# Performance work log

Measured on AMD Instinct MI355X. Metric: run time of the kernel, lower is better.

The kernel has to match this reference:

```python
import jax, jax.numpy as jnp
import numpy as np

H, DH, DIM = 8, 64, 512
GAMMA, LAMBDA_REG = 0.01, 0.001


def setup_inputs() -> dict:
    key = jax.random.key(0)
    ks = jax.random.split(key, 12)
    Q, N = 4, 1024
    f = lambda k, shape, s=0.02: jax.random.normal(k, shape, dtype=jnp.float32) * s
    return {
        "q": jax.random.normal(ks[0], (Q, N, DIM), dtype=jnp.float32),
        "k": jax.random.normal(ks[1], (Q, N, DIM), dtype=jnp.float32),
        "v": jax.random.normal(ks[2], (Q, N, DIM), dtype=jnp.float32),
        "ln_w": jnp.ones((DIM,), jnp.float32),
        "ln_b": jnp.zeros((DIM,), jnp.float32),
        "W_in": f(ks[3], (DIM, H * DH)),
        "W_out": f(ks[4], (H * DH, DIM)),
        "b_out": jnp.zeros((DIM,), jnp.float32),
        "wp_W1": f(ks[5], (2 * DH, 4 * DH), 0.05),
        "wp_b1": jnp.zeros((4 * DH,), jnp.float32),
        "wp_ln_w": jnp.ones((4 * DH,), jnp.float32),
        "wp_ln_b": jnp.zeros((4 * DH,), jnp.float32),
        "wp_W2": f(ks[6], (4 * DH, 3 * DH), 0.05),
        "wp_b2": jnp.zeros((3 * DH,), jnp.float32),
        "wp_W3": f(ks[7], (3 * DH, DH), 0.05),
        "wp_b3": jnp.zeros((DH,), jnp.float32),
        "wp_W4": f(ks[8], (DH, 3), 0.05),
        "wp_b4": jnp.zeros((3,), jnp.float32),
        "weight_temp": jnp.ones((1,), jnp.float32) * 0.1,
    }


def _layernorm(x, w, b, eps=1e-5):
    mu = x.mean(-1, keepdims=True)
    var = x.var(-1, keepdims=True)  # biased, matches torch LayerNorm
    return (x - mu) / jnp.sqrt(var + eps) * w + b


def reference(q, k, v, ln_w, ln_b, W_in, W_out, b_out,
              wp_W1, wp_b1, wp_ln_w, wp_ln_b, wp_W2, wp_b2,
              wp_W3, wp_b3, wp_W4, wp_b4, weight_temp):
    # input_linear: LN -> Linear(no bias) -> (dropout=identity in eval)
    def proj(t):
        x = _layernorm(t, ln_w, ln_b) @ W_in  # [Q, N, H*DH]
        Qn, Nn = x.shape[0], x.shape[1]
        return x.reshape(Qn, Nn, H, DH).transpose(2, 0, 1, 3)  # h q n d

    fq, fk, fv = proj(q), proj(k), proj(v)
    m = fk.shape[2]

    # --- cosine component (cosine_distance + extra clamp) ---
    raw = jnp.einsum('hqnd,hqmd->hqnm', fq, fk)
    n1 = jnp.linalg.norm(fq, axis=-1)[..., :, None] + 1e-6
    n2 = jnp.linalg.norm(fk, axis=-1)[..., None, :] + 1e-6
    cosine_sim = jnp.clip(raw / (n1 * n2), -0.95, 0.95)

    # --- regularized covariance component ---
    fkc = fk - fk.mean(axis=2, keepdims=True)       # center keys over token dim
    fqc = fq - fq.mean(axis=-1, keepdims=True)      # center queries over feature dim
    cov = jnp.einsum('hqnd,hqmd->hqnm', fqc, fkc) / (DH ** 0.5 + 1e-4)
    cov = jnp.clip((LAMBDA_REG / max(m, 1)) * cov, -50.0, 50.0)

    # --- margin-based variance component (eval: adaptive_gamma = gamma) ---
    fqn = fq / jnp.maximum(jnp.linalg.norm(fq, axis=-1, keepdims=True), 1e-4)
    fkn = fk / jnp.maximum(jnp.linalg.norm(fk, axis=-1, keepdims=True), 1e-4)
    cs = jnp.clip(jnp.einsum('hqnd,hqmd->hqnm', fqn, fkn), -0.95, 0.95)
    margin = jnp.clip(GAMMA - cs, 0.0, 15.0)
    var_comp = jnp.broadcast_to(margin.mean(-1, keepdims=True), cs.shape)

    # --- dynamic per-head weights via MLP predictor ---
    feat = jnp.concatenate([fq.mean(axis=(1, 2)), fk.mean(axis=(1, 2))], axis=-1)  # (h, 2*DH)
    h1 = jax.nn.relu(_layernorm(feat @ wp_W1 + wp_b1, wp_ln_w, wp_ln_b))
    h2 = jax.nn.relu(h1 @ wp_W2 + wp_b2)
    h3 = jax.nn.relu(h2 @ wp_W3 + wp_b3)
    probs = jax.nn.softmax(h3 @ wp_W4 + wp_b4, axis=-1)  # predictor ends in Softmax
    wt = jnp.clip(weight_temp, 0.01, 1.0)
    w = jax.nn.softmax(probs / wt, axis=-1)
    w = jnp.clip(w, 0.01, 0.95)
    w = w / w.sum(-1, keepdims=True)
    cos_w = w[:, 0].reshape(H, 1, 1, 1)
    cov_w = w[:, 1].reshape(H, 1, 1, 1)
    var_w = w[:, 2].reshape(H, 1, 1, 1)

    # --- std-normalized weighted combination (torch.std is unbiased, detached) ---
    sg = jax.lax.stop_gradient
    ustd = lambda x: jnp.std(x, ddof=1)
    dots = (cos_w * (cosine_sim / (sg(ustd(cosine_sim)) + 1e-4))
            + cov_w * (cov / (sg(ustd(cov)) + 1e-4) * 0.3)
            + var_w * (var_comp / (sg(ustd(var_comp)) + 1e-4) * 0.3))

    ds = ustd(dots)  # NOT detached in original
    temp = jnp.where(ds < 1e-5, 0.01, jnp.where(ds < 1e-3, 0.05, 0.2 + ds * 2.0))
    temp = jnp.clip(temp, 0.01, 8.0)

    attn = jax.nn.softmax(dots / temp, axis=-1)
    out = jnp.einsum('hqnm,hqmd->hqnd', attn, fv)
    out = out.transpose(1, 2, 0, 3).reshape(out.shape[1], out.shape[2], H * DH)  # q n (h d)
    return out @ W_out + b_out
```

## Files before the change

kernel.cpp:

```cpp
#include <hip/hip_runtime.h>
#include <math.h>

typedef _Float16 f16;
typedef _Float16 v8h __attribute__((ext_vector_type(8)));
typedef _Float16 v4h __attribute__((ext_vector_type(4)));
typedef float    v4f __attribute__((ext_vector_type(4)));

#define MFMA(a, b, c) __builtin_amdgcn_mfma_f32_16x16x32_f16((a), (b), (c), 0, 0, 0)

#define OFF_LN16    0u
#define OFF_FQ16    4194304u
#define OFF_FK16    5242880u
#define OFF_FVHT    6291456u
#define OFF_WINTH   8388608u
#define OFF_WOUTTH  8650752u
#define OFF_AVH     8912896u
#define OFF_AVL     9961472u
#define OFF_RQ1     11010048u
#define OFF_RQ2     11042816u
#define OFF_MUQ     11075584u
#define OFF_RK1     11108352u
#define OFF_RK2     11141120u
#define OFF_SK      11173888u
#define OFF_VC      11206656u
#define OFF_ROWCOS  11272192u
#define OFF_ROWCOV  11337728u
#define OFF_NUACC   11403264u
#define OFF_PB      11405312u
#define OFF_HS      11411456u
#define OFF_RP      11411520u
#define OFF_FEAT    11411712u
#define OFF_WV      11412736u
#define OFF_SCAL    11412760u
#define OFF_MAXC    11412768u
#define OFF_MAXV    11478304u

__device__ __forceinline__ float clampf(float x, float lo, float hi) {
    return fminf(fmaxf(x, lo), hi);
}

__global__ void k_zero(float* feat, float* nuacck) {
    int i = blockIdx.x * 256 + threadIdx.x;
    if (i < 1024) feat[i] = 0.0f;
    if (i < 2048) nuacck[i] = 0.0f;
}

__global__ __launch_bounds__(256) void k_wprep(const float* __restrict__ Win,
        const float* __restrict__ Wout, f16* __restrict__ WinTh,
        f16* __restrict__ WoutTh) {
    __shared__ float lds[64][68];
    const float* W = blockIdx.z ? Wout : Win;
    f16* Th = blockIdx.z ? WoutTh : WinTh;
    int k0 = blockIdx.y * 64, c0 = blockIdx.x * 64;
    int t = threadIdx.x;
    #pragma unroll
    for (int p = 0; p < 4; ++p) {
        int flat = p * 1024 + t * 4;
        int r = flat >> 6, c = flat & 63;
        *(float4*)&lds[r][c] = *(const float4*)&W[(size_t)(k0 + r) * 512 + c0 + c];
    }
    __syncthreads();
    int c = t >> 2, kk = (t & 3) * 16;
    #pragma unroll
    for (int half = 0; half < 2; ++half) {
        v8h h8;
        #pragma unroll
        for (int ii = 0; ii < 8; ++ii)
            h8[ii] = (f16)lds[kk + half * 8 + ii][c];
        *(v8h*)&Th[(size_t)(c0 + c) * 512 + k0 + kk + half * 8] = h8;
    }
}

__global__ __launch_bounds__(256) void k_ln16(const float* __restrict__ q,
        const float* __restrict__ kk, const float* __restrict__ v,
        const float* __restrict__ lnw, const float* __restrict__ lnb,
        f16* __restrict__ ln16) {
    int t = threadIdx.x, wid = t >> 6, lane = t & 63;
    int token = blockIdx.x * 4 + wid;
    int inp = token >> 12, lt = token & 4095;
    const float* xp = (inp == 0) ? q : ((inp == 1) ? kk : v);
    const float4* xr = (const float4*)(xp + (size_t)lt * 512);
    float4 a = xr[lane], b = xr[lane + 64];
    float s = a.x + a.y + a.z + a.w + b.x + b.y + b.z + b.w;
    float s2 = a.x*a.x + a.y*a.y + a.z*a.z + a.w*a.w
             + b.x*b.x + b.y*b.y + b.z*b.z + b.w*b.w;
    for (int o = 32; o > 0; o >>= 1) { s += __shfl_down(s, o); s2 += __shfl_down(s2, o); }
    float m_ = __shfl(s, 0) * (1.0f / 512.0f);
    float var = __shfl(s2, 0) * (1.0f / 512.0f) - m_ * m_;
    var = fmaxf(var, 0.0f);
    float rs = rsqrtf(var + 1e-5f);
    const float4* w4 = (const float4*)lnw;
    const float4* b4 = (const float4*)lnb;
    float4 wa = w4[lane], wb = w4[lane + 64], ba = b4[lane], bb = b4[lane + 64];
    f16* orow = ln16 + (size_t)token * 512;
    v4h ha, hb;
    ha[0] = (f16)((a.x - m_) * rs * wa.x + ba.x);
    ha[1] = (f16)((a.y - m_) * rs * wa.y + ba.y);
    ha[2] = (f16)((a.z - m_) * rs * wa.z + ba.z);
    ha[3] = (f16)((a.w - m_) * rs * wa.w + ba.w);
    hb[0] = (f16)((b.x - m_) * rs * wb.x + bb.x);
    hb[1] = (f16)((b.y - m_) * rs * wb.y + bb.y);
    hb[2] = (f16)((b.z - m_) * rs * wb.z + bb.z);
    hb[3] = (f16)((b.w - m_) * rs * wb.w + bb.w);
    *(v4h*)&orow[lane * 4] = ha;
    *(v4h*)&orow[lane * 4 + 256] = hb;
}

template<int MODE>
__device__ __forceinline__ void proj_body(const f16* __restrict__ A16,
        const f16* __restrict__ BTh,
        f16* __restrict__ fout16, f16* __restrict__ fhT,
        float* __restrict__ oA, float* __restrict__ oB, float* __restrict__ oC,
        float* __restrict__ feat, float* __restrict__ nuacck) {
    int t = threadIdx.x, l = t & 63, w = t >> 6;
    int wr = w >> 1, wc = w & 1;
    int col0 = blockIdx.x * 128 + wc * 64;
    int tok0 = blockIdx.y * 128 + wr * 64;
    int lr = l & 15, kg = (l >> 4) * 8;
    int rg4 = (l >> 4) * 4;
    v4f acc[4][4] = {};
    for (int ks = 0; ks < 512; ks += 32) {
        v8h a[4], b[4];
        #pragma unroll
        for (int i = 0; i < 4; ++i)
            a[i] = *(const v8h*)&A16[(size_t)(tok0 + i * 16 + lr) * 512 + ks + kg];
        #pragma unroll
        for (int j = 0; j < 4; ++j)
            b[j] = *(const v8h*)&BTh[(size_t)(col0 + j * 16 + lr) * 512 + ks + kg];
        #pragma unroll
        for (int i = 0; i < 4; ++i)
            #pragma unroll
            for (int j = 0; j < 4; ++j)
                acc[i][j] = MFMA(a[i], b[j], acc[i][j]);
    }
    int h = col0 >> 6;
    #pragma unroll
    for (int i = 0; i < 4; ++i)
        #pragma unroll
        for (int j = 0; j < 4; ++j)
            #pragma unroll
            for (int r = 0; r < 4; ++r) {
                int token = tok0 + i * 16 + rg4 + r;
                int d = j * 16 + lr;
                int qi = token >> 10, n = token & 1023;
                float val = acc[i][j][r];
                if constexpr (MODE != 2) {
                    fout16[((size_t)((h << 2) + qi) * 1024 + n) * 64 + d] = (f16)val;
                } else {
                    fhT[((size_t)((h << 2) + qi) * 64 + d) * 1024 + n] = (f16)val;
                }
            }
    if constexpr (MODE != 2) {
        #pragma unroll
        for (int i = 0; i < 4; ++i)
            #pragma unroll
            for (int r = 0; r < 4; ++r) {
                float s = 0.f, s2 = 0.f;
                #pragma unroll
                for (int j = 0; j < 4; ++j) { float v = acc[i][j][r]; s += v; s2 += v * v; }
                #pragma unroll
                for (int mk = 1; mk <= 8; mk <<= 1) {
                    s += __shfl_xor(s, mk); s2 += __shfl_xor(s2, mk);
                }
                if (lr == 0) {
                    int token = tok0 + i * 16 + rg4 + r;
                    int qi = token >> 10, n = token & 1023;
                    int row = ((h << 2) + qi) * 1024 + n;
                    float nv = sqrtf(s2);
                    oA[row] = 1.0f / (nv + 1e-6f);
                    oB[row] = 1.0f / fmaxf(nv, 1e-4f);
                    oC[row] = (MODE == 0) ? s * (1.0f / 64.0f) : s;
                }
            }
        float cs[4];
        #pragma unroll
        for (int j = 0; j < 4; ++j) {
            float c = 0.f;
            #pragma unroll
            for (int i = 0; i < 4; ++i)
                #pragma unroll
                for (int r = 0; r < 4; ++r) c += acc[i][j][r];
            c += __shfl_xor(c, 16); c += __shfl_xor(c, 32);
            cs[j] = c;
        }
        if (l < 16) {
            #pragma unroll
            for (int j = 0; j < 4; ++j)
                atomicAdd(&feat[h * 128 + (MODE == 1 ? 64 : 0) + j * 16 + l],
                          cs[j] * (1.0f / 4096.0f));
            if constexpr (MODE == 1) {
                int qi = tok0 >> 10;
                #pragma unroll
                for (int j = 0; j < 4; ++j)
                    atomicAdd(&nuacck[((h << 2) + qi) * 64 + j * 16 + l], cs[j]);
            }
        }
    }
}

__global__ __launch_bounds__(256) void k_proj_all(const f16* __restrict__ ln16,
        const f16* __restrict__ BTh,
        f16* __restrict__ fq16, f16* __restrict__ fk16,
        f16* __restrict__ fvhT,
        float* __restrict__ rq1, float* __restrict__ rq2, float* __restrict__ muq,
        float* __restrict__ rk1, float* __restrict__ rk2, float* __restrict__ sk,
        float* __restrict__ feat, float* __restrict__ nuacck) {
    int mode = blockIdx.z;
    if (mode == 0)
        proj_body<0>(ln16, BTh, fq16, nullptr, rq1, rq2, muq, feat, nullptr);
    else if (mode == 1)
        proj_body<1>(ln16 + 2097152u, BTh, fk16, nullptr, rk1, rk2, sk, feat, nuacck);
    else
        proj_body<2>(ln16 + 4194304u, BTh, nullptr, fvhT,
                     nullptr, nullptr, nullptr, nullptr, nullptr);
}

__global__ __launch_bounds__(256) void k_mlp(const float* __restrict__ feat,
        const float* __restrict__ W1, const float* __restrict__ b1,
        const float* __restrict__ lw, const float* __restrict__ lb,
        const float* __restrict__ W2, const float* __restrict__ b2,
        const float* __restrict__ W3, const float* __restrict__ b3,
        const float* __restrict__ W4, const float* __restrict__ b4,
        const float* __restrict__ wtemp, float* wv) {
    __shared__ float h1[256], h2[192], h3[64], red[8];
    int t = threadIdx.x;
    int h = blockIdx.x;
    float p = 0.0f;
    for (int i = 0; i < 128; ++i) p += feat[h * 128 + i] * W1[i * 256 + t];
    p += b1[t];
    float s = p, s2 = p * p;
    for (int o = 32; o > 0; o >>= 1) { s += __shfl_down(s, o); s2 += __shfl_down(s2, o); }
    if ((t & 63) == 0) { red[t >> 6] = s; red[4 + (t >> 6)] = s2; }
    __syncthreads();
    float S = red[0] + red[1] + red[2] + red[3];
    float S2 = red[4] + red[5] + red[6] + red[7];
    float mu = S / 256.0f;
    float var = S2 / 256.0f - mu * mu; if (var < 0.0f) var = 0.0f;
    float xh = (p - mu) * rsqrtf(var + 1e-5f) * lw[t] + lb[t];
    h1[t] = fmaxf(xh, 0.0f);
    __syncthreads();
    if (t < 192) {
        float a = 0.0f;
        for (int i = 0; i < 256; ++i) a += h1[i] * W2[i * 192 + t];
        h2[t] = fmaxf(a + b2[t], 0.0f);
    }
    __syncthreads();
    if (t < 64) {
        float a = 0.0f;
        for (int i = 0; i < 192; ++i) a += h2[i] * W3[i * 64 + t];
        h3[t] = fmaxf(a + b3[t], 0.0f);
    }
    __syncthreads();
    if (t == 0) {
        float lg[3];
        for (int j = 0; j < 3; ++j) {
            float a = 0.0f;
            for (int i = 0; i < 64; ++i) a += h3[i] * W4[i * 3 + j];
            lg[j] = a + b4[j];
        }
        float mx = fmaxf(lg[0], fmaxf(lg[1], lg[2]));
        float e0 = expf(lg[0] - mx), e1 = expf(lg[1] - mx), e2 = expf(lg[2] - mx);
        float se = e0 + e1 + e2;
        float pr0 = e0 / se, pr1 = e1 / se, pr2 = e2 / se;
        float wt = wtemp[0]; wt = fminf(fmaxf(wt, 0.01f), 1.0f);
        float q0 = pr0 / wt, q1 = pr1 / wt, q2 = pr2 / wt;
        float m2 = fmaxf(q0, fmaxf(q1, q2));
        float f0 = expf(q0 - m2), f1 = expf(q1 - m2), f2 = expf(q2 - m2);
        float sf = f0 + f1 + f2; f0 /= sf; f1 /= sf; f2 /= sf;
        f0 = fminf(fmaxf(f0, 0.01f), 0.95f);
        f1 = fminf(fmaxf(f1, 0.01f), 0.95f);
        f2 = fminf(fmaxf(f2, 0.01f), 0.95f);
        float sw = f0 + f1 + f2;
        wv[h * 3 + 0] = f0 / sw; wv[h * 3 + 1] = f1 / sw; wv[h * 3 + 2] = f2 / sw;
    }
}

#define PASS_PREAMBLE_AB                                                       \
    int hq = blockIdx.z;                                                       \
    int half = blockIdx.y;                                                     \
    int m0base = half * 512;                                                   \
    int t = threadIdx.x, l = t & 63, w = t >> 6;                               \
    int lr = l & 15, kg = (l >> 4) * 8, rg4 = (l >> 4) * 4;                    \
    int nb = blockIdx.x * 64 + w * 16;                                         \
    const f16* Q = fq16 + (size_t)hq * 65536;                                  \
    const f16* K = fk16 + (size_t)hq * 65536;                                  \
    v8h aq0 = *(const v8h*)&Q[(size_t)(nb + lr) * 64 + kg];                    \
    v8h aq1 = *(const v8h*)&Q[(size_t)(nb + lr) * 64 + 32 + kg];               \
    const float inv1024 = 1.0f / 1024.0f;                                      \
    float uvp = nuacck[hq * 64 + l] * inv1024;                                 \
    _Pragma("unroll")                                                          \
    for (int o = 32; o > 0; o >>= 1) uvp += __shfl_xor(uvp, o);                \
    float uv = uvp;                                                            \
    float tp = 0.f;                                                            \
    _Pragma("unroll")                                                          \
    for (int e = 0; e < 8; ++e)                                                \
        tp += (float)aq0[e] * nuacck[hq * 64 + kg + e]                         \
            + (float)aq1[e] * nuacck[hq * 64 + 32 + kg + e];                   \
    tp *= inv1024;                                                             \
    tp += __shfl_xor(tp, 16);                                                  \
    tp += __shfl_xor(tp, 32);                                                  \
    float muv[4], tv[4];                                                       \
    _Pragma("unroll")                                                          \
    for (int r = 0; r < 4; ++r) {                                              \
        muv[r] = muq[hq * 1024 + nb + rg4 + r];                                \
        tv[r] = __shfl(tp, rg4 + r);                                           \
    }                                                                          \
    const float Acs = (0.001f / 1024.0f) / 8.0001f;                            \
    float Pr[4], Gr[4];                                                        \
    _Pragma("unroll")                                                          \
    for (int r = 0; r < 4; ++r) {                                              \
        Gr[r] = Acs * muv[r];                                                  \
        Pr[r] = Acs * fmaf(muv[r], uv, -tv[r]);                                \
    }

#define LOAD_KTILE(m0a)                                                        \
    v8h b0[4], b1[4];                                                          \
    _Pragma("unroll")                                                          \
    for (int j = 0; j < 4; ++j) {                                              \
        b0[j] = *(const v8h*)&K[(size_t)((m0a) + j * 16 + lr) * 64 + kg];      \
        b1[j] = *(const v8h*)&K[(size_t)((m0a) + j * 16 + lr) * 64 + 32 + kg]; \
    }

__global__ __launch_bounds__(256) void k_passA(const f16* __restrict__ fq16,
        const f16* __restrict__ fk16, const float* __restrict__ rq1,
        const float* __restrict__ rq2, const float* __restrict__ muq,
        const float* __restrict__ rk1, const float* __restrict__ rk2,
        const float* __restrict__ sk, const float* __restrict__ nuacck,
        float* __restrict__ vcrow, float* __restrict__ rowcos,
        float* __restrict__ rowcov, float* __restrict__ maxc,
        float* __restrict__ maxv, float* __restrict__ pb) {
    __shared__ float rk1s[512], rk2s[512], sks[512];
    PASS_PREAMBLE_AB
    {
        int i2 = t * 2;
        *(float2*)&rk1s[i2] = *(const float2*)&rk1[hq * 1024 + m0base + i2];
        *(float2*)&rk2s[i2] = *(const float2*)&rk2[hq * 1024 + m0base + i2];
        *(float2*)&sks[i2]  = *(const float2*)&sk[hq * 1024 + m0base + i2];
    }
    __syncthreads();
    float rq1v[4], rq2v[4];
    #pragma unroll
    for (int r = 0; r < 4; ++r) {
        rq1v[r] = rq1[hq * 1024 + nb + rg4 + r];
        rq2v[r] = rq2[hq * 1024 + nb + rg4 + r];
    }
    float scos = 0, s2cos = 0, scov = 0, s2cov = 0, sccov = 0;
    float mp[4] = {}, rcs[4] = {}, rcv[4] = {};
    float mcs[4] = { -1e30f, -1e30f, -1e30f, -1e30f };
    float mcv[4] = { -1e30f, -1e30f, -1e30f, -1e30f };
    #pragma unroll 2
    for (int m0 = 0; m0 < 512; m0 += 64) {
        LOAD_KTILE(m0base + m0)
        float rk1v[4], rk2v[4], skv[4];
        #pragma unroll
        for (int j = 0; j < 4; ++j) {
            int cg = m0 + j * 16 + lr;
            rk1v[j] = rk1s[cg]; rk2v[j] = rk2s[cg]; skv[j] = sks[cg];
        }
        v4f acc[4] = {};
        #pragma unroll
        for (int j = 0; j < 4; ++j) {
            acc[j] = MFMA(aq0, b0[j], acc[j]);
            acc[j] = MFMA(aq1, b1[j], acc[j]);
        }
        #pragma unroll
        for (int j = 0; j < 4; ++j)
            #pragma unroll
            for (int r = 0; r < 4; ++r) {
                float rv = acc[j][r];
                float cosv = clampf(rv * rq1v[r] * rk1v[j], -0.95f, 0.95f);
                float x2 = rv * rq2v[r] * rk2v[j];
                float marg = fmaxf(0.01f - fmaxf(x2, -0.95f), 0.0f);
                float cov = fmaf(-Gr[r], skv[j], fmaf(Acs, rv, Pr[r]));
                scos += cosv; s2cos = fmaf(cosv, cosv, s2cos);
                scov += cov;  s2cov = fmaf(cov, cov, s2cov);
                sccov = fmaf(cosv, cov, sccov);
                mp[r] += marg; rcs[r] += cosv; rcv[r] += cov;
                mcs[r] = fmaxf(mcs[r], cosv);
                mcv[r] = fmaxf(mcv[r], cov);
            }
    }
    #pragma unroll
    for (int r = 0; r < 4; ++r) {
        float m_ = mp[r], c_ = rcs[r], v_ = rcv[r];
        float xc = mcs[r], xv = mcv[r];
        #pragma unroll
        for (int mk = 1; mk <= 8; mk <<= 1) {
            m_ += __shfl_xor(m_, mk);
            c_ += __shfl_xor(c_, mk);
            v_ += __shfl_xor(v_, mk);
            xc = fmaxf(xc, __shfl_xor(xc, mk));
            xv = fmaxf(xv, __shfl_xor(xv, mk));
        }
        if (lr == 0) {
            int row = hq * 1024 + nb + rg4 + r;
            vcrow[half * 32768 + row] = m_ * inv1024;
            rowcos[half * 32768 + row] = c_;
            rowcov[half * 32768 + row] = v_;
            maxc[half * 32768 + row] = xc;
            maxv[half * 32768 + row] = xv;
        }
    }
    for (int o = 32; o > 0; o >>= 1) {
        scos += __shfl_down(scos, o); s2cos += __shfl_down(s2cos, o);
        scov += __shfl_down(scov, o); s2cov += __shfl_down(s2cov, o);
        sccov += __shfl_down(sccov, o);
    }
    __shared__ float bs[4][5];
    if (l == 0) { bs[w][0] = scos; bs[w][1] = s2cos; bs[w][2] = scov;
                  bs[w][3] = s2cov; bs[w][4] = sccov; }
    __syncthreads();
    if (t == 0) {
        int bid = (hq * 2 + half) * 16 + blockIdx.x;
        #pragma unroll
        for (int s = 0; s < 5; ++s)
            pb[bid * 6 + s] = bs[0][s] + bs[1][s] + bs[2][s] + bs[3][s];
    }
}

__global__ __launch_bounds__(256) void k_fin1(const float* __restrict__ pb,
        const float* __restrict__ vcrow, float* __restrict__ hs,
        float* __restrict__ scal) {
    __shared__ float hsl[40];
    int t = threadIdx.x;
    int hd = t >> 5, idx = t & 31;
    double a0 = 0, a1 = 0, a2 = 0, a3 = 0, a4 = 0;
    for (int i = idx; i < 128; i += 32) {
        const float* p = &pb[(hd * 128 + i) * 6];
        a0 += p[0]; a1 += p[1]; a2 += p[2]; a3 += p[3]; a4 += p[4];
    }
    for (int m = 1; m <= 16; m <<= 1) {
        a0 += __shfl_xor(a0, m); a1 += __shfl_xor(a1, m); a2 += __shfl_xor(a2, m);
        a3 += __shfl_xor(a3, m); a4 += __shfl_xor(a4, m);
    }
    if (idx == 0) {
        hsl[hd * 5 + 0] = (float)a0; hsl[hd * 5 + 1] = (float)a1;
        hsl[hd * 5 + 2] = (float)a2; hsl[hd * 5 + 3] = (float)a3;
        hsl[hd * 5 + 4] = (float)a4;
        hs[hd * 5 + 0] = (float)a0; hs[hd * 5 + 1] = (float)a1;
        hs[hd * 5 + 2] = (float)a2; hs[hd * 5 + 3] = (float)a3;
        hs[hd * 5 + 4] = (float)a4;
    }
    double s4 = 0, s5 = 0;
    for (int i = t; i < 32768; i += 256) {
        double rm = (double)(vcrow[i] + vcrow[32768 + i]);
        s4 += rm; s5 += rm * rm;
    }
    for (int o = 32; o > 0; o >>= 1) { s4 += __shfl_down(s4, o); s5 += __shfl_down(s5, o); }
    __shared__ double red[2][4];
    int wid = t >> 6, lane = t & 63;
    if (lane == 0) { red[0][wid] = s4; red[1][wid] = s5; }
    __syncthreads();
    if (t == 0) {
        double S4 = red[0][0] + red[0][1] + red[0][2] + red[0][3];
        double S5 = red[1][0] + red[1][1] + red[1][2] + red[1][3];
        double S0 = 0, S1 = 0, S2 = 0, S3 = 0;
        for (int h2 = 0; h2 < 8; ++h2) {
            S0 += hsl[h2 * 5 + 0]; S1 += hsl[h2 * 5 + 1];
            S2 += hsl[h2 * 5 + 2]; S3 += hsl[h2 * 5 + 3];
        }
        const double cnt = 33554432.0;
        scal[0] = (float)sqrt(fmax(0.0, (S1 - S0 * S0 / cnt) / (cnt - 1.0)));
        scal[1] = (float)sqrt(fmax(0.0, (S3 - S2 * S2 / cnt) / (cnt - 1.0)));
        double V4 = S4 * 1024.0, V5 = S5 * 1024.0;
        scal[2] = (float)sqrt(fmax(0.0, (V5 - V4 * V4 / cnt) / (cnt - 1.0)));
    }
}

__global__ __launch_bounds__(256) void k_finrow(const float* __restrict__ vcrow,
        const float* __restrict__ rowcos, const float* __restrict__ rowcov,
        const float* __restrict__ wv, const float* __restrict__ scal,
        float* __restrict__ rp) {
    int t = threadIdx.x;
    float s1 = scal[0] + 1e-4f, s2v = scal[1] + 1e-4f, s3 = scal[2] + 1e-4f;
    float p1 = 0, p2 = 0, p3 = 0;
    #pragma unroll
    for (int i = 0; i < 2; ++i) {
        int row = blockIdx.x * 512 + i * 256 + t;
        int h = row >> 12;
        float fc1 = wv[h * 3] / s1;
        float fc2 = wv[h * 3 + 1] * 0.3f / s2v;
        float c3 = wv[h * 3 + 2] * 0.3f / s3;
        float a = (vcrow[row] + vcrow[32768 + row]) * c3;
        float b = fc1 * (rowcos[row] + rowcos[32768 + row])
                + fc2 * (rowcov[row] + rowcov[32768 + row]);
        p1 += a; p2 = fmaf(a, a, p2); p3 = fmaf(a, b, p3);
    }
    for (int o = 32; o > 0; o >>= 1) {
        p1 += __shfl_down(p1, o); p2 += __shfl_down(p2, o); p3 += __shfl_down(p3, o);
    }
    __shared__ float red[3][4];
    int wid = t >> 6, lane = t & 63;
    if (lane == 0) { red[0][wid] = p1; red[1][wid] = p2; red[2][wid] = p3; }
    __syncthreads();
    if (t == 0) {
        rp[blockIdx.x * 3 + 0] = red[0][0] + red[0][1] + red[0][2] + red[0][3];
        rp[blockIdx.x * 3 + 1] = red[1][0] + red[1][1] + red[1][2] + red[1][3];
        rp[blockIdx.x * 3 + 2] = red[2][0] + red[2][1] + red[2][2] + red[2][3];
    }
}

__global__ __launch_bounds__(64) void k_fin2(const float* __restrict__ rp,
        const float* __restrict__ hs, const float* __restrict__ wv,
        float* __restrict__ scal) {
    int t = threadIdx.x;
    double p1 = rp[t * 3 + 0], p2 = rp[t * 3 + 1], p3 = rp[t * 3 + 2];
    for (int o = 32; o > 0; o >>= 1) {
        p1 += __shfl_down(p1, o); p2 += __shfl_down(p2, o); p3 += __shfl_down(p3, o);
    }
    if (t == 0) {
        double s1 = (double)scal[0] + 1e-4, s2v = (double)scal[1] + 1e-4;
        double sdd = 1024.0 * p1;
        double sdd2 = 2.0 * p3 + 1024.0 * p2;
        for (int h = 0; h < 8; ++h) {
            double fc1 = (double)wv[h * 3] / s1;
            double fc2 = (double)wv[h * 3 + 1] * 0.3 / s2v;
            sdd += fc1 * hs[h * 5 + 0] + fc2 * hs[h * 5 + 2];
            sdd2 += fc1 * fc1 * hs[h * 5 + 1] + fc2 * fc2 * hs[h * 5 + 3]
                  + 2.0 * fc1 * fc2 * hs[h * 5 + 4];
        }
        const double cnt = 33554432.0;
        double ds = sqrt(fmax(0.0, (sdd2 - sdd * sdd / cnt) / (cnt - 1.0)));
        float temp = (ds < 1e-5) ? 0.01f : ((ds < 1e-3) ? 0.05f : (0.2f + (float)ds * 2.0f));
        temp = fminf(fmaxf(temp, 0.01f), 8.0f);
        scal[3] = temp;
    }
}

#define TILE_STEP(PBASE, MK)                                                   \
    {                                                                          \
        int mk = (MK);                                                         \
        v8h b0[4], b1[4];                                                      \
        _Pragma("unroll")                                                      \
        for (int j = 0; j < 4; ++j) {                                          \
            b0[j] = *(const v8h*)&K[(size_t)(mk + j * 16 + lr) * 64 + kg];     \
            b1[j] = *(const v8h*)&K[(size_t)(mk + j * 16 + lr) * 64 + 32 + kg];\
        }                                                                      \
        float rk1v[4], skv[4];                                                 \
        _Pragma("unroll")                                                      \
        for (int j = 0; j < 4; ++j) {                                          \
            int cg = mk + j * 16 + lr;                                         \
            rk1v[j] = rk1s[cg]; skv[j] = sks[cg];                              \
        }                                                                      \
        v4f acc[4] = {};                                                       \
        _Pragma("unroll")                                                      \
        for (int j = 0; j < 4; ++j) {                                          \
            acc[j] = MFMA(aq0, b0[j], acc[j]);                                 \
            acc[j] = MFMA(aq1, b1[j], acc[j]);                                 \
        }                                                                      \
        _Pragma("unroll")                                                      \
        for (int j = 0; j < 4; ++j)                                            \
            _Pragma("unroll")                                                  \
            for (int r = 0; r < 4; ++r) {                                      \
                float rv = acc[j][r];                                          \
                float cosv = clampf(rv * rq1v[r] * rk1v[j], -0.95f, 0.95f);    \
                float cov = fmaf(-Gcr[r], skv[j], fmaf(Acs, rv, Pcr[r]));      \
                float d2 = fmaf(fc2, cov, fmaf(fc1, cosv, addc[r]));           \
                float pe = __expf(fmaf(d2, invt, -mxr[r]));                    \
                f16 p16 = (f16)pe;                                             \
                rsacc[r] += (float)p16;                                        \
                (PBASE)[(w * 16 + rg4 + r) * 72 + j * 16 + lr] = p16;          \
            }                                                                  \
        v8h pa0 = *(const v8h*)&(PBASE)[(w * 16 + lr) * 72 + kg];              \
        v8h pa1 = *(const v8h*)&(PBASE)[(w * 16 + lr) * 72 + 32 + kg];         \
        _Pragma("unroll")                                                      \
        for (int j = 0; j < 4; ++j) {                                          \
            size_t vb = ((size_t)hq * 64 + j * 16 + lr) * 1024 + mk;           \
            v8h vh0 = *(const v8h*)&fvhT[vb + kg];                             \
            v8h vh1 = *(const v8h*)&fvhT[vb + 32 + kg];                        \
            accpv[j] = MFMA(pa0, vh0, accpv[j]);                               \
            accpv[j] = MFMA(pa1, vh1, accpv[j]);                               \
        }                                                                      \
    }

__global__ __launch_bounds__(512) void k_passC(const f16* __restrict__ fq16,
        const f16* __restrict__ fk16, const float* __restrict__ rq1,
        const float* __restrict__ muq, const float* __restrict__ rk1,
        const float* __restrict__ sk, const float* __restrict__ nuacck,
        const float* __restrict__ vcrow, const float* __restrict__ maxca,
        const float* __restrict__ maxva, const float* __restrict__ wv,
        const float* __restrict__ scal,
        const f16* __restrict__ fvhT,
        f16* __restrict__ avh, f16* __restrict__ avl) {
    __shared__ __align__(16) char arena[36864];
    __shared__ float rk1s[1024], sks[1024];
    f16* Pa = (f16*)arena;
    f16* Pb = (f16*)(arena + 18432);
    int hq = blockIdx.y;
    int t = threadIdx.x, l = t & 63, w = t >> 6;
    int rg = w & 3, kh = w >> 2;
    int lr = l & 15, kg = (l >> 4) * 8, rg4 = (l >> 4) * 4;
    int nb = blockIdx.x * 64 + rg * 16;
    int m0base = kh * 512;
    const f16* Q = fq16 + (size_t)hq * 65536;
    const f16* K = fk16 + (size_t)hq * 65536;
    {
        int i2 = t * 2;
        *(float2*)&rk1s[i2] = *(const float2*)&rk1[hq * 1024 + i2];
        *(float2*)&sks[i2]  = *(const float2*)&sk[hq * 1024 + i2];
    }
    __syncthreads();
    v8h aq0 = *(const v8h*)&Q[(size_t)(nb + lr) * 64 + kg];
    v8h aq1 = *(const v8h*)&Q[(size_t)(nb + lr) * 64 + 32 + kg];
    const float inv1024 = 1.0f / 1024.0f;
    float uvp = nuacck[hq * 64 + l] * inv1024;
    #pragma unroll
    for (int o = 32; o > 0; o >>= 1) uvp += __shfl_xor(uvp, o);
    float uv = uvp;
    float tpv = 0.f;
    #pragma unroll
    for (int e = 0; e < 8; ++e)
        tpv += (float)aq0[e] * nuacck[hq * 64 + kg + e]
             + (float)aq1[e] * nuacck[hq * 64 + 32 + kg + e];
    tpv *= inv1024;
    tpv += __shfl_xor(tpv, 16);
    tpv += __shfl_xor(tpv, 32);
    float muv[4], tv[4];
    #pragma unroll
    for (int r = 0; r < 4; ++r) {
        muv[r] = muq[hq * 1024 + nb + rg4 + r];
        tv[r] = __shfl(tpv, rg4 + r);
    }
    const float Acs = (0.001f / 1024.0f) / 8.0001f;
    float Pcr[4], Gcr[4];
    #pragma unroll
    for (int r = 0; r < 4; ++r) {
        Gcr[r] = Acs * muv[r];
        Pcr[r] = Acs * fmaf(muv[r], uv, -tv[r]);
    }
    int h = hq >> 2;
    float s1 = scal[0] + 1e-4f, s2v = scal[1] + 1e-4f, s3 = scal[2] + 1e-4f;
    float fc1 = wv[h * 3] / s1;
    float fc2 = wv[h * 3 + 1] * 0.3f / s2v;
    float c3 = wv[h * 3 + 2] * 0.3f / s3;
    float invt = 1.0f / scal[3];
    float rq1v[4], addc[4], mxr[4];
    #pragma unroll
    for (int r = 0; r < 4; ++r) {
        int row = hq * 1024 + nb + rg4 + r;
        rq1v[r] = rq1[row];
        addc[r] = (vcrow[row] + vcrow[32768 + row]) * c3;
        float mc = fmaxf(maxca[row], maxca[32768 + row]);
        float mv = fmaxf(maxva[row], maxva[32768 + row]);
        mxr[r] = fmaf(fc1, mc, fmaf(fc2, mv, addc[r])) * invt;
    }
    v4f accpv[4] = {};
    float rsacc[4] = {};
    for (int it = 0; it < 4; ++it) {
        TILE_STEP(Pa, m0base + it * 128)
        TILE_STEP(Pb, m0base + it * 128 + 64)
    }
    __syncthreads();
    #pragma unroll
    for (int r = 0; r < 4; ++r) {
        float s = rsacc[r];
        s += __shfl_xor(s, 1); s += __shfl_xor(s, 2);
        s += __shfl_xor(s, 4); s += __shfl_xor(s, 8);
        rsacc[r] = s;
    }
    float* cbacc = (float*)arena;
    float* cbrs  = (float*)(arena + 16384);
    if (kh == 1) {
        #pragma unroll
        for (int j = 0; j < 4; ++j)
            #pragma unroll
            for (int r = 0; r < 4; ++r)
                cbacc[(rg * 16 + j * 4 + r) * 64 + l] = accpv[j][r];
        #pragma unroll
        for (int r = 0; r < 4; ++r) cbrs[(rg * 4 + r) * 64 + l] = rsacc[r];
    }
    __syncthreads();
    if (kh == 0) {
        float rinv[4];
        #pragma unroll
        for (int r = 0; r < 4; ++r)
            rinv[r] = 1.0f / (rsacc[r] + cbrs[(rg * 4 + r) * 64 + l]);
        #pragma unroll
        for (int j = 0; j < 4; ++j)
            #pragma unroll
            for (int r = 0; r < 4; ++r) {
                float val = (accpv[j][r] + cbacc[(rg * 16 + j * 4 + r) * 64 + l])
                            * rinv[r];
                size_t idx = ((size_t)(hq * 1024 + nb + rg4 + r)) * 64 + j * 16 + lr;
                f16 hi = (f16)val;
                avh[idx] = hi;
                avl[idx] = (f16)(val - (float)hi);
            }
    }
}

__global__ __launch_bounds__(256) void k_out_mfma(const f16* __restrict__ avh,
        const f16* __restrict__ avl,
        const f16* __restrict__ WoutTh,
        const float* __restrict__ bout, float* __restrict__ out) {
    __shared__ float red[2][4][4][4][64];
    int t = threadIdx.x, l = t & 63, w = t >> 6;
    int wc = w & 1, kh = w >> 1;
    int col0 = blockIdx.x * 128 + wc * 64;
    int tok0 = blockIdx.y * 64;
    int qi = tok0 >> 10, nb = tok0 & 1023;
    int lr = l & 15, kg = (l >> 4) * 8;
    v4f acc[4][4] = {};
    for (int ks8 = 0; ks8 < 8; ++ks8) {
        int ks = kh * 256 + ks8 * 32;
        int f = ks + kg;
        int h = f >> 6, d = f & 63;
        size_t hb = (size_t)((h << 2) + qi) * 1024;
        v8h ah[4], al4[4], bh[4];
        #pragma unroll
        for (int i = 0; i < 4; ++i) {
            int n = nb + i * 16 + lr;
            ah[i]  = *(const v8h*)&avh[(hb + n) * 64 + d];
            al4[i] = *(const v8h*)&avl[(hb + n) * 64 + d];
        }
        #pragma unroll
        for (int j = 0; j < 4; ++j)
            bh[j] = *(const v8h*)&WoutTh[(size_t)(col0 + j * 16 + lr) * 512 + ks + kg];
        #pragma unroll
        for (int i = 0; i < 4; ++i)
            #pragma unroll
            for (int j = 0; j < 4; ++j) {
                acc[i][j] = MFMA(ah[i], bh[j], acc[i][j]);
                acc[i][j] = MFMA(al4[i], bh[j], acc[i][j]);
            }
    }
    if (kh == 0) {
        #pragma unroll
        for (int i = 0; i < 4; ++i)
            #pragma unroll
            for (int j = 0; j < 4; ++j)
                #pragma unroll
                for (int r = 0; r < 4; ++r)
                    red[wc][i][j][r][l] = acc[i][j][r];
    }
    __syncthreads();
    if (kh == 1) {
        #pragma unroll
        for (int i = 0; i < 4; ++i)
            #pragma unroll
            for (int j = 0; j < 4; ++j) {
                int col = col0 + j * 16 + lr;
                float bo = bout[col];
                #pragma unroll
                for (int r = 0; r < 4; ++r) {
                    float val = acc[i][j][r] + red[wc][i][j][r][l] + bo;
                    int token = tok0 + i * 16 + (l >> 4) * 4 + r;
                    out[(size_t)token * 512 + col] = val;
                }
            }
    }
}

extern "C" void kernel_launch(void* const* d_in, const int* in_sizes, int n_in,
                              void* d_out, int out_size, void* d_ws, size_t ws_size,
                              hipStream_t stream) {
    const float* q     = (const float*)d_in[0];
    const float* k     = (const float*)d_in[1];
    const float* v     = (const float*)d_in[2];
    const float* ln_w  = (const float*)d_in[3];
    const float* ln_b  = (const float*)d_in[4];
    const float* W_in  = (const float*)d_in[5];
    const float* W_out = (const float*)d_in[6];
    const float* b_out = (const float*)d_in[7];
    const float* wp_W1 = (const float*)d_in[8];
    const float* wp_b1 = (const float*)d_in[9];
    const float* wp_lw = (const float*)d_in[10];
    const float* wp_lb = (const float*)d_in[11];
    const float* wp_W2 = (const float*)d_in[12];
    const float* wp_b2 = (const float*)d_in[13];
    const float* wp_W3 = (const float*)d_in[14];
    const float* wp_b3 = (const float*)d_in[15];
    const float* wp_W4 = (const float*)d_in[16];
    const float* wp_b4 = (const float*)d_in[17];
    const float* wtemp = (const float*)d_in[18];

    float* ws = (float*)d_ws;
    f16* ln16     = (f16*)(ws + OFF_LN16);
    f16* fq16     = (f16*)(ws + OFF_FQ16);
    f16* fk16     = (f16*)(ws + OFF_FK16);
    f16* fvhT     = (f16*)(ws + OFF_FVHT);
    f16* WinTh    = (f16*)(ws + OFF_WINTH);
    f16* WoutTh   = (f16*)(ws + OFF_WOUTTH);
    f16* avh      = (f16*)(ws + OFF_AVH);
    f16* avl      = (f16*)(ws + OFF_AVL);
    float* rq1    = ws + OFF_RQ1;
    float* rq2    = ws + OFF_RQ2;
    float* muq    = ws + OFF_MUQ;
    float* rk1    = ws + OFF_RK1;
    float* rk2    = ws + OFF_RK2;
    float* sk     = ws + OFF_SK;
    float* vcrow  = ws + OFF_VC;
    float* rowcos = ws + OFF_ROWCOS;
    float* rowcov = ws + OFF_ROWCOV;
    float* maxc   = ws + OFF_MAXC;
    float* maxv   = ws + OFF_MAXV;
    float* nuacck = ws + OFF_NUACC;
    float* pb     = ws + OFF_PB;
    float* hs     = ws + OFF_HS;
    float* rp     = ws + OFF_RP;
    float* feat   = ws + OFF_FEAT;
    float* wv     = ws + OFF_WV;
    float* scal   = ws + OFF_SCAL;

    k_zero<<<8, 256, 0, stream>>>(feat, nuacck);
    k_wprep<<<dim3(8, 8, 2), 256, 0, stream>>>(W_in, W_out, WinTh, WoutTh);
    k_ln16<<<3072, 256, 0, stream>>>(q, k, v, ln_w, ln_b, ln16);
    k_proj_all<<<dim3(4, 32, 3), 256, 0, stream>>>(ln16, WinTh,
            fq16, fk16, fvhT, rq1, rq2, muq, rk1, rk2, sk, feat, nuacck);
    k_mlp<<<8, 256, 0, stream>>>(feat, wp_W1, wp_b1, wp_lw, wp_lb,
                                 wp_W2, wp_b2, wp_W3, wp_b3, wp_W4, wp_b4,
                                 wtemp, wv);
    k_passA<<<dim3(16, 2, 32), 256, 0, stream>>>(fq16, fk16, rq1, rq2, muq, rk1, rk2,
                                                 sk, nuacck, vcrow, rowcos, rowcov,
                                                 maxc, maxv, pb);
    k_fin1<<<1, 256, 0, stream>>>(pb, vcrow, hs, scal);
    k_finrow<<<64, 256, 0, stream>>>(vcrow, rowcos, rowcov, wv, scal, rp);
    k_fin2<<<1, 64, 0, stream>>>(rp, hs, wv, scal);
    k_passC<<<dim3(16, 32), 512, 0, stream>>>(fq16, fk16, rq1, muq, rk1, sk, nuacck,
                                              vcrow, maxc, maxv, wv, scal,
                                              fvhT, avh, avl);
    k_out_mfma<<<dim3(4, 64), 256, 0, stream>>>(avh, avl, WoutTh, b_out,
                                                (float*)d_out);
}
```

Measured before the change: 248.7 us.

## Drop fp16 lo-split for attention output, fold softmax constants into exp2, trim passA sums

The attention-output activations are now stored as a single fp16 value instead of a hi/lo fp16 pair, which halves the output-projection MFMAs and the avh/avl traffic. In passC, the temperature, log2e, the cov coefficients and the row max are folded into per-row constants, so each score takes fewer FMAs and uses exp2f. In passA, the global cos/cov sums are rebuilt from the per-row sums instead of being accumulated separately. The fp16-only output projection gives up precision that the hi/lo split used to keep.

```diff
diff --git a/kernel.cpp b/kernel.cpp
--- a/kernel.cpp
+++ b/kernel.cpp
@@ -15,7 +15,6 @@
 #define OFF_WINTH   8388608u
 #define OFF_WOUTTH  8650752u
 #define OFF_AVH     8912896u
-#define OFF_AVL     9961472u
 #define OFF_RQ1     11010048u
 #define OFF_RQ2     11042816u
 #define OFF_MUQ     11075584u
@@ -344,7 +343,7 @@
         rq1v[r] = rq1[hq * 1024 + nb + rg4 + r];
         rq2v[r] = rq2[hq * 1024 + nb + rg4 + r];
     }
-    float scos = 0, s2cos = 0, scov = 0, s2cov = 0, sccov = 0;
+    float s2cos = 0, s2cov = 0, sccov = 0;
     float mp[4] = {}, rcs[4] = {}, rcv[4] = {};
     float mcs[4] = { -1e30f, -1e30f, -1e30f, -1e30f };
     float mcv[4] = { -1e30f, -1e30f, -1e30f, -1e30f };
@@ -372,14 +371,16 @@
                 float x2 = rv * rq2v[r] * rk2v[j];
                 float marg = fmaxf(0.01f - fmaxf(x2, -0.95f), 0.0f);
                 float cov = fmaf(-Gr[r], skv[j], fmaf(Acs, rv, Pr[r]));
-                scos += cosv; s2cos = fmaf(cosv, cosv, s2cos);
-                scov += cov;  s2cov = fmaf(cov, cov, s2cov);
+                s2cos = fmaf(cosv, cosv, s2cos);
+                s2cov = fmaf(cov, cov, s2cov);
                 sccov = fmaf(cosv, cov, sccov);
                 mp[r] += marg; rcs[r] += cosv; rcv[r] += cov;
                 mcs[r] = fmaxf(mcs[r], cosv);
                 mcv[r] = fmaxf(mcv[r], cov);
             }
     }
+    float scos = rcs[0] + rcs[1] + rcs[2] + rcs[3];
+    float scov = rcv[0] + rcv[1] + rcv[2] + rcv[3];
     #pragma unroll
     for (int r = 0; r < 4; ++r) {
         float m_ = mp[r], c_ = rcs[r], v_ = rcv[r];
@@ -554,9 +555,9 @@
             for (int r = 0; r < 4; ++r) {                                      \
                 float rv = acc[j][r];                                          \
                 float cosv = clampf(rv * rq1v[r] * rk1v[j], -0.95f, 0.95f);    \
-                float cov = fmaf(-Gcr[r], skv[j], fmaf(Acs, rv, Pcr[r]));      \
-                float d2 = fmaf(fc2, cov, fmaf(fc1, cosv, addc[r]));           \
-                float pe = __expf(fmaf(d2, invt, -mxr[r]));                    \
+                float arg = fmaf(fc1s, cosv,                                   \
+                              fmaf(-G2[r], skv[j], fmaf(A2, rv, Cr[r])));      \
+                float pe = exp2f(arg);                                         \
                 f16 p16 = (f16)pe;                                             \
                 rsacc[r] += (float)p16;                                        \
                 (PBASE)[(w * 16 + rg4 + r) * 72 + j * 16 + lr] = p16;          \
@@ -581,7 +582,7 @@
         const float* __restrict__ maxva, const float* __restrict__ wv,
         const float* __restrict__ scal,
         const f16* __restrict__ fvhT,
-        f16* __restrict__ avh, f16* __restrict__ avl) {
+        f16* __restrict__ avh) {
     __shared__ __align__(16) char arena[36864];
     __shared__ float rk1s[1024], sks[1024];
     f16* Pa = (f16*)arena;
@@ -622,27 +623,26 @@
         tv[r] = __shfl(tpv, rg4 + r);
     }
     const float Acs = (0.001f / 1024.0f) / 8.0001f;
-    float Pcr[4], Gcr[4];
-    #pragma unroll
-    for (int r = 0; r < 4; ++r) {
-        Gcr[r] = Acs * muv[r];
-        Pcr[r] = Acs * fmaf(muv[r], uv, -tv[r]);
-    }
     int h = hq >> 2;
     float s1 = scal[0] + 1e-4f, s2v = scal[1] + 1e-4f, s3 = scal[2] + 1e-4f;
     float fc1 = wv[h * 3] / s1;
     float fc2 = wv[h * 3 + 1] * 0.3f / s2v;
     float c3 = wv[h * 3 + 2] * 0.3f / s3;
-    float invt = 1.0f / scal[3];
-    float rq1v[4], addc[4], mxr[4];
+    const float LOG2E = 1.44269504088896f;
+    float sfold = (1.0f / scal[3]) * LOG2E;
+    float fc1s = fc1 * sfold;
+    float A2 = fc2 * Acs * sfold;
+    float rq1v[4], G2[4], Cr[4];
     #pragma unroll
     for (int r = 0; r < 4; ++r) {
         int row = hq * 1024 + nb + rg4 + r;
         rq1v[r] = rq1[row];
-        addc[r] = (vcrow[row] + vcrow[32768 + row]) * c3;
+        float addc = (vcrow[row] + vcrow[32768 + row]) * c3;
         float mc = fmaxf(maxca[row], maxca[32768 + row]);
         float mv = fmaxf(maxva[row], maxva[32768 + row]);
-        mxr[r] = fmaf(fc1, mc, fmaf(fc2, mv, addc[r])) * invt;
+        float Pcr = Acs * fmaf(muv[r], uv, -tv[r]);
+        G2[r] = fc2 * Acs * muv[r] * sfold;
+        Cr[r] = (fc2 * Pcr - fc1 * mc - fc2 * mv) * sfold;
     }
     v4f accpv[4] = {};
     float rsacc[4] = {};
@@ -682,15 +682,12 @@
                 float val = (accpv[j][r] + cbacc[(rg * 16 + j * 4 + r) * 64 + l])
                             * rinv[r];
                 size_t idx = ((size_t)(hq * 1024 + nb + rg4 + r)) * 64 + j * 16 + lr;
-                f16 hi = (f16)val;
-                avh[idx] = hi;
-                avl[idx] = (f16)(val - (float)hi);
+                avh[idx] = (f16)val;
             }
     }
 }
 
 __global__ __launch_bounds__(256) void k_out_mfma(const f16* __restrict__ avh,
-        const f16* __restrict__ avl,
         const f16* __restrict__ WoutTh,
         const float* __restrict__ bout, float* __restrict__ out) {
     __shared__ float red[2][4][4][4][64];
@@ -706,12 +703,11 @@
         int f = ks + kg;
         int h = f >> 6, d = f & 63;
         size_t hb = (size_t)((h << 2) + qi) * 1024;
-        v8h ah[4], al4[4], bh[4];
+        v8h ah[4], bh[4];
         #pragma unroll
         for (int i = 0; i < 4; ++i) {
             int n = nb + i * 16 + lr;
-            ah[i]  = *(const v8h*)&avh[(hb + n) * 64 + d];
-            al4[i] = *(const v8h*)&avl[(hb + n) * 64 + d];
+            ah[i] = *(const v8h*)&avh[(hb + n) * 64 + d];
         }
         #pragma unroll
         for (int j = 0; j < 4; ++j)
@@ -719,10 +715,8 @@
         #pragma unroll
         for (int i = 0; i < 4; ++i)
             #pragma unroll
-            for (int j = 0; j < 4; ++j) {
+            for (int j = 0; j < 4; ++j)
                 acc[i][j] = MFMA(ah[i], bh[j], acc[i][j]);
-                acc[i][j] = MFMA(al4[i], bh[j], acc[i][j]);
-            }
     }
     if (kh == 0) {
         #pragma unroll
@@ -782,7 +776,6 @@
     f16* WinTh    = (f16*)(ws + OFF_WINTH);
     f16* WoutTh   = (f16*)(ws + OFF_WOUTTH);
     f16* avh      = (f16*)(ws + OFF_AVH);
-    f16* avl      = (f16*)(ws + OFF_AVL);
     float* rq1    = ws + OFF_RQ1;
     float* rq2    = ws + OFF_RQ2;
     float* muq    = ws + OFF_MUQ;
@@ -818,7 +811,7 @@
     k_fin2<<<1, 64, 0, stream>>>(rp, hs, wv, scal);
     k_passC<<<dim3(16, 32), 512, 0, stream>>>(fq16, fk16, rq1, muq, rk1, sk, nuacck,
                                               vcrow, maxc, maxv, wv, scal,
-                                              fvhT, avh, avl);
-    k_out_mfma<<<dim3(4, 64), 256, 0, stream>>>(avh, avl, WoutTh, b_out,
+                                              fvhT, avh);
+    k_out_mfma<<<dim3(4, 64), 256, 0, stream>>>(avh, WoutTh, b_out,
                                                 (float*)d_out);
 }
```

After: 241.4 us. -2.9%, faster.
